# Optimization experiments

Hardware: AMD Instinct MI355X
Metric: run time of the kernel (lower is better)

## Reference

```python
import jax, jax.numpy as jnp
import numpy as np

KNOTS = 17  # integration points on [0, 3]


def _buffers():
    t = jnp.linspace(0.0, 3.0, KNOTS, dtype=jnp.float32)
    dt = 3.0 / (KNOTS - 1)
    w = jnp.full((KNOTS,), 2.0 * dt, dtype=jnp.float32)
    w = w.at[0].set(dt).at[-1].set(dt)          # trapezoid-style end weights
    phi = jnp.exp(-jnp.square(t) / 2.0)         # ideal Gaussian ECF
    return t, phi, w * phi


def setup_inputs() -> dict:
    key = jax.random.key(0)
    k1, k2 = jax.random.split(key)
    N, D, P = 8192, 512, 1024
    z = jax.random.normal(k1, (N, D), dtype=jnp.float32)
    A = jax.random.normal(k2, (D, P), dtype=jnp.float32)  # random projections (hoisted from forward)
    return {"z": z, "A": A}


def reference(z, A):
    t, phi, weights = _buffers()
    D = z.shape[-1]
    flat = z.reshape(-1, D).astype(jnp.float32)            # [N, D]
    An = A / jnp.clip(jnp.linalg.norm(A, axis=0, keepdims=True), 1e-8)
    proj = flat @ An                                       # [N, P]
    x_t = proj[:, :, None] * t                             # [N, P, K]
    cos_mean = jnp.mean(jnp.cos(x_t), axis=0)              # [P, K]
    sin_mean = jnp.mean(jnp.sin(x_t), axis=0)              # [P, K]
    err = jnp.square(cos_mean - phi) + jnp.square(sin_mean)
    statistic = (err @ weights) * flat.shape[0]            # [P]
    return jnp.mean(statistic)
```

## Files before the change

### kernel.cpp

```cpp
#include <hip/hip_runtime.h>
#include <stdint.h>

#define N_SAMP 8192
#define D_DIM  512
#define P_DIM  1024
#define DT     0.1875f

typedef float f32x4 __attribute__((ext_vector_type(4)));
typedef float f32x2 __attribute__((ext_vector_type(2)));
typedef short bf16x8 __attribute__((ext_vector_type(8)));
typedef unsigned short u16;

__device__ __forceinline__ u16 f2bf(float x){
    unsigned int u = __float_as_uint(x);
    return (u16)((u + 0x7FFFu + ((u >> 16) & 1u)) >> 16);
}

__device__ __forceinline__ void load_lds16(const void* g, void* l){
    __builtin_amdgcn_global_load_lds(
        (const __attribute__((address_space(1))) void*)(uintptr_t)g,
        (__attribute__((address_space(3))) void*)(uint32_t)(uintptr_t)l,
        16, 0, 0);
}

__global__ __launch_bounds__(256) void k_prep0(const float4* __restrict__ z4,
                                               u16* __restrict__ zb,
                                               const float* __restrict__ A,
                                               float* __restrict__ inv,
                                               float* __restrict__ out){
    const int tid = threadIdx.x;
    if (blockIdx.x < 4096){
        int i = blockIdx.x * 256 + tid;
        if (i == 0) out[0] = 0.f;
        float4 v = z4[i];
        ushort4 o;
        o.x = f2bf(v.x); o.y = f2bf(v.y); o.z = f2bf(v.z); o.w = f2bf(v.w);
        ((ushort4*)zb)[i] = o;
        return;
    }
    __shared__ float red[8][32];
    const int p0 = (blockIdx.x - 4096) * 32;
    const int pl = tid & 31, dg = tid >> 5;
    float s = 0.f;
    #pragma unroll 8
    for (int i = 0; i < 64; ++i){
        float v = A[(size_t)(dg + 8 * i) * P_DIM + p0 + pl];
        s += v * v;
    }
    red[dg][pl] = s;
    __syncthreads();
    if (tid < 32){
        float t = 0.f;
        #pragma unroll
        for (int g = 0; g < 8; ++g) t += red[g][tid];
        inv[p0 + tid] = 1.0f / fmaxf(sqrtf(t), 1e-8f);
    }
}

__global__ __launch_bounds__(256) void k_trans(const float* __restrict__ A,
                                               const float* __restrict__ inv,
                                               u16* __restrict__ AnT){
    __shared__ float tile[32][33];
    int p0 = (blockIdx.x & 31) * 32;
    int d0 = (blockIdx.x >> 5) * 32;
    int tx = threadIdx.x & 31, ty = threadIdx.x >> 5;
    #pragma unroll
    for (int j = 0; j < 4; ++j){
        int dd = ty + j * 8;
        tile[dd][tx] = A[(size_t)(d0 + dd) * P_DIM + p0 + tx];
    }
    __syncthreads();
    #pragma unroll
    for (int j = 0; j < 4; ++j){
        int pp = ty + j * 8;
        float s = inv[p0 + pp];
        AnT[(size_t)(p0 + pp) * D_DIM + d0 + tx] = f2bf(tile[tx][pp] * s);
    }
}

__global__ __launch_bounds__(256) void k_gemm_ecf(const u16* __restrict__ zb,
                                                  const u16* __restrict__ AnT,
                                                  float* __restrict__ partial){
    __shared__ uint4 smem4[4096];
    const int tid = threadIdx.x;
    const int swz = (blockIdx.x & 7) * 64 + (blockIdx.x >> 3);
    const int bm = swz >> 3, bn = swz & 7;
    const int m0 = bm << 7, n0 = bn << 7;
    const int w = tid >> 6, lane = tid & 63;
    const int r = lane & 15, kg = lane >> 4;
    const int wm = (w >> 1) << 6, wn = (w & 1) << 6;

    const int srow = tid >> 3;
    const int gsw  = ((tid & 7) ^ (srow & 7)) << 3;
    const u16* gA = zb  + (size_t)(m0 + srow) * D_DIM + gsw;
    const u16* gB = AnT + (size_t)(n0 + srow) * D_DIM + gsw;
    char* lbase = (char*)smem4 + w * 1024;

    f32x4 acc[4][4] = {};

    #pragma unroll
    for (int i = 0; i < 4; ++i){
        load_lds16(gA + (size_t)i * 32 * D_DIM, lbase + i * 4096);
        load_lds16(gB + (size_t)i * 32 * D_DIM, lbase + 16384 + i * 4096);
    }

    for (int kt = 0; kt < 8; ++kt){
        const int cur = kt & 1;
        __syncthreads();
        if (kt < 7){
            char* la = lbase + ((kt + 1) & 1) * 32768;
            #pragma unroll
            for (int i = 0; i < 4; ++i){
                load_lds16(gA + (size_t)i * 32 * D_DIM + (kt + 1) * 64, la + i * 4096);
                load_lds16(gB + (size_t)i * 32 * D_DIM + (kt + 1) * 64, la + 16384 + i * 4096);
            }
        }
        const u16* Ab = (const u16*)smem4 + cur * 16384;
        const u16* Bb = Ab + 8192;
        #pragma unroll
        for (int ks = 0; ks < 2; ++ks){
            bf16x8 af[4], bfr[4];
            #pragma unroll
            for (int i = 0; i < 4; ++i)
                af[i] = *(const bf16x8*)&Ab[(wm + i * 16 + r) * 64 +
                                            (((ks * 4 + kg) ^ (r & 7)) << 3)];
            #pragma unroll
            for (int j = 0; j < 4; ++j)
                bfr[j] = *(const bf16x8*)&Bb[(wn + j * 16 + r) * 64 +
                                             (((ks * 4 + kg) ^ (r & 7)) << 3)];
            #pragma unroll
            for (int i = 0; i < 4; ++i)
                #pragma unroll
                for (int j = 0; j < 4; ++j)
                    acc[i][j] = __builtin_amdgcn_mfma_f32_16x16x32_bf16(
                        af[i], bfr[j], acc[i][j], 0, 0, 0);
        }
    }

    __syncthreads();
    float* epil = (float*)smem4;
    #pragma unroll
    for (int jn = 0; jn < 4; ++jn){
        f32x2 sum[16];
        #pragma unroll
        for (int k = 0; k < 16; ++k) sum[k] = (f32x2){0.f, 0.f};
        #pragma unroll
        for (int i = 0; i < 4; ++i){
            #pragma unroll
            for (int q = 0; q < 4; ++q){
                float x = acc[i][jn][q] * DT;
                float c1 = __cosf(x), s1 = __sinf(x);
                float tc = c1 + c1;
                f32x2 prev = {1.f, 0.f};
                f32x2 curv = {c1, s1};
                sum[0] += curv;
                #pragma unroll
                for (int k = 2; k <= 16; ++k){
                    f32x2 nxt = tc * curv - prev;
                    sum[k - 1] += nxt;
                    prev = curv; curv = nxt;
                }
            }
        }
        #pragma unroll
        for (int k = 0; k < 16; ++k){
            f32x2 o;
            o.x = __shfl_xor(sum[k].x, 16); o.y = __shfl_xor(sum[k].y, 16);
            sum[k] += o;
            o.x = __shfl_xor(sum[k].x, 32); o.y = __shfl_xor(sum[k].y, 32);
            sum[k] += o;
        }
        if (lane < 16){
            const int cl = jn * 16 + lane;
            #pragma unroll
            for (int k = 0; k < 16; ++k){
                epil[(w * 32 + k)      * 64 + cl] = sum[k].x;
                epil[(w * 32 + 16 + k) * 64 + cl] = sum[k].y;
            }
        }
    }
    __syncthreads();
    for (int f0 = 0; f0 < 4096; f0 += 256){
        int f = f0 + tid;
        int cl = f & 127, j = f >> 7;
        int whi = cl >> 6, cll = cl & 63;
        float v = epil[(whi * 32 + j) * 64 + cll] +
                  epil[((whi + 2) * 32 + j) * 64 + cll];
        partial[((size_t)bm * 32 + j) * 1024 + n0 + cl] = v;
    }
}

__global__ __launch_bounds__(256) void k_reduce(const float* __restrict__ partial,
                                                float* __restrict__ out){
    const int tid = threadIdx.x;
    const int gt = blockIdx.x * 256 + tid;
    const int pair = gt >> 2, quarter = gt & 3;
    const int p = pair & 1023, j = pair >> 10;
    float s = 0.f;
    #pragma unroll
    for (int i = 0; i < 16; ++i)
        s += partial[((size_t)(quarter * 16 + i) * 32 + j) * 1024 + p];
    s += __shfl_xor(s, 1);
    s += __shfl_xor(s, 2);
    const int k = (j & 15) + 1;
    float tk = (float)k * DT;
    float phik = expf(-0.5f * tk * tk);
    float wk = ((k == 16) ? DT : 2.f * DT) * phik;
    float mean = s * (1.f / (float)N_SAMP);
    float diff = (j < 16) ? (mean - phik) : mean;
    float term = diff * diff * wk;
    #pragma unroll
    for (int o = 32; o > 0; o >>= 1) term += __shfl_xor(term, o);
    __shared__ float red[4];
    if ((tid & 63) == 0) red[tid >> 6] = term;
    __syncthreads();
    if (tid == 0)
        atomicAdd(out, (red[0] + red[1] + red[2] + red[3]) * 0.25f *
                       ((float)N_SAMP / (float)P_DIM));
}

extern "C" void kernel_launch(void* const* d_in, const int* in_sizes, int n_in,
                              void* d_out, int out_size, void* d_ws, size_t ws_size,
                              hipStream_t stream){
    const float* z = (const float*)d_in[0];
    const float* A = (const float*)d_in[1];
    char* ws = (char*)d_ws;
    float* inv     = (float*)(ws);
    u16*   AnT     = (u16*)  (ws + 8192);
    u16*   zb      = (u16*)  (ws + 1056768);
    float* partial = (float*)(ws + 9445376);
    float* out     = (float*)d_out;

    hipLaunchKernelGGL(k_prep0,    dim3(4128), dim3(256), 0, stream,
                       (const float4*)z, zb, A, inv, out);
    hipLaunchKernelGGL(k_trans,    dim3(512),  dim3(256), 0, stream, A, inv, AnT);
    hipLaunchKernelGGL(k_gemm_ecf, dim3(512),  dim3(256), 0, stream, zb, AnT, partial);
    hipLaunchKernelGGL(k_reduce,   dim3(512),  dim3(256), 0, stream, partial, out);
}
```

Before: 50.86 us.

## Fuse prep kernels, defer column scaling to epilogue, reduce partials with atomics

Folds the norm computation, transpose to bf16 and zeroing of the accumulation buffer into one prep launch. The transpose no longer waits on the norms because the per-column inverse norm is now applied in the GEMM epilogue. The per-row-block partial sums are atomically added into a single 32x1024 buffer, so the final reduce reads 128K floats instead of 2M and runs 128 blocks. This removes one launch and a large partial write/read. In exchange it adds atomic contention (64 adders per address), makes the summation order nondeterministic, and bf16-rounds the unnormalized A.

```diff
diff --git a/kernel.cpp b/kernel.cpp
--- a/kernel.cpp
+++ b/kernel.cpp
@@ -23,14 +23,17 @@
         16, 0, 0);
 }
 
-__global__ __launch_bounds__(256) void k_prep0(const float4* __restrict__ z4,
-                                               u16* __restrict__ zb,
-                                               const float* __restrict__ A,
-                                               float* __restrict__ inv,
-                                               float* __restrict__ out){
+__global__ __launch_bounds__(256) void k_prep(const float4* __restrict__ z4,
+                                              u16* __restrict__ zb,
+                                              const float* __restrict__ A,
+                                              float* __restrict__ inv,
+                                              u16* __restrict__ AnT,
+                                              float* __restrict__ gpart,
+                                              float* __restrict__ out){
     const int tid = threadIdx.x;
-    if (blockIdx.x < 4096){
-        int i = blockIdx.x * 256 + tid;
+    const int b = blockIdx.x;
+    if (b < 4096){
+        int i = b * 256 + tid;
         if (i == 0) out[0] = 0.f;
         float4 v = z4[i];
         ushort4 o;
@@ -38,49 +41,50 @@
         ((ushort4*)zb)[i] = o;
         return;
     }
-    __shared__ float red[8][32];
-    const int p0 = (blockIdx.x - 4096) * 32;
-    const int pl = tid & 31, dg = tid >> 5;
-    float s = 0.f;
-    #pragma unroll 8
-    for (int i = 0; i < 64; ++i){
-        float v = A[(size_t)(dg + 8 * i) * P_DIM + p0 + pl];
-        s += v * v;
-    }
-    red[dg][pl] = s;
-    __syncthreads();
-    if (tid < 32){
-        float t = 0.f;
-        #pragma unroll
-        for (int g = 0; g < 8; ++g) t += red[g][tid];
-        inv[p0 + tid] = 1.0f / fmaxf(sqrtf(t), 1e-8f);
-    }
-}
-
-__global__ __launch_bounds__(256) void k_trans(const float* __restrict__ A,
-                                               const float* __restrict__ inv,
-                                               u16* __restrict__ AnT){
-    __shared__ float tile[32][33];
-    int p0 = (blockIdx.x & 31) * 32;
-    int d0 = (blockIdx.x >> 5) * 32;
-    int tx = threadIdx.x & 31, ty = threadIdx.x >> 5;
-    #pragma unroll
-    for (int j = 0; j < 4; ++j){
-        int dd = ty + j * 8;
-        tile[dd][tx] = A[(size_t)(d0 + dd) * P_DIM + p0 + tx];
-    }
-    __syncthreads();
-    #pragma unroll
-    for (int j = 0; j < 4; ++j){
-        int pp = ty + j * 8;
-        float s = inv[p0 + pp];
-        AnT[(size_t)(p0 + pp) * D_DIM + d0 + tx] = f2bf(tile[tx][pp] * s);
-    }
+    if (b < 4128){
+        __shared__ float red[8][32];
+        const int p0 = (b - 4096) * 32;
+        const int pl = tid & 31, dg = tid >> 5;
+        float s = 0.f;
+        #pragma unroll 8
+        for (int i = 0; i < 64; ++i){
+            float v = A[(size_t)(dg + 8 * i) * P_DIM + p0 + pl];
+            s += v * v;
+        }
+        red[dg][pl] = s;
+        __syncthreads();
+        if (tid < 32){
+            float t = 0.f;
+            #pragma unroll
+            for (int g = 0; g < 8; ++g) t += red[g][tid];
+            inv[p0 + tid] = 1.0f / fmaxf(sqrtf(t), 1e-8f);
+        }
+        return;
+    }
+    if (b < 4640){
+        __shared__ float tile[32][33];
+        const int t = b - 4128;
+        const int p0 = (t & 31) * 32, d0 = (t >> 5) * 32;
+        const int tx = tid & 31, ty = tid >> 5;
+        #pragma unroll
+        for (int j = 0; j < 4; ++j)
+            tile[ty + j * 8][tx] = A[(size_t)(d0 + ty + j * 8) * P_DIM + p0 + tx];
+        __syncthreads();
+        #pragma unroll
+        for (int j = 0; j < 4; ++j){
+            int pp = ty + j * 8;
+            AnT[(size_t)(p0 + pp) * D_DIM + d0 + tx] = f2bf(tile[tx][pp]);
+        }
+        return;
+    }
+    int i = (b - 4640) * 256 + tid;
+    ((float4*)gpart)[i] = (float4){0.f, 0.f, 0.f, 0.f};
 }
 
 __global__ __launch_bounds__(256) void k_gemm_ecf(const u16* __restrict__ zb,
                                                   const u16* __restrict__ AnT,
-                                                  float* __restrict__ partial){
+                                                  const float* __restrict__ inv,
+                                                  float* __restrict__ gpart){
     __shared__ uint4 smem4[4096];
     const int tid = threadIdx.x;
     const int swz = (blockIdx.x & 7) * 64 + (blockIdx.x >> 3);
@@ -141,6 +145,7 @@
     float* epil = (float*)smem4;
     #pragma unroll
     for (int jn = 0; jn < 4; ++jn){
+        const float sc = inv[n0 + wn + jn * 16 + r] * DT;
         f32x2 sum[16];
         #pragma unroll
         for (int k = 0; k < 16; ++k) sum[k] = (f32x2){0.f, 0.f};
@@ -148,7 +153,7 @@
         for (int i = 0; i < 4; ++i){
             #pragma unroll
             for (int q = 0; q < 4; ++q){
-                float x = acc[i][jn][q] * DT;
+                float x = acc[i][jn][q] * sc;
                 float c1 = __cosf(x), s1 = __sinf(x);
                 float tc = c1 + c1;
                 f32x2 prev = {1.f, 0.f};
@@ -186,22 +191,16 @@
         int whi = cl >> 6, cll = cl & 63;
         float v = epil[(whi * 32 + j) * 64 + cll] +
                   epil[((whi + 2) * 32 + j) * 64 + cll];
-        partial[((size_t)bm * 32 + j) * 1024 + n0 + cl] = v;
-    }
-}
-
-__global__ __launch_bounds__(256) void k_reduce(const float* __restrict__ partial,
+        atomicAdd(&gpart[j * P_DIM + n0 + cl], v);
+    }
+}
+
+__global__ __launch_bounds__(256) void k_reduce(const float* __restrict__ gpart,
                                                 float* __restrict__ out){
     const int tid = threadIdx.x;
-    const int gt = blockIdx.x * 256 + tid;
-    const int pair = gt >> 2, quarter = gt & 3;
-    const int p = pair & 1023, j = pair >> 10;
-    float s = 0.f;
-    #pragma unroll
-    for (int i = 0; i < 16; ++i)
-        s += partial[((size_t)(quarter * 16 + i) * 32 + j) * 1024 + p];
-    s += __shfl_xor(s, 1);
-    s += __shfl_xor(s, 2);
+    const int idx = blockIdx.x * 256 + tid;
+    const int j = idx >> 10;
+    float s = gpart[idx];
     const int k = (j & 15) + 1;
     float tk = (float)k * DT;
     float phik = expf(-0.5f * tk * tk);
@@ -215,7 +214,7 @@
     if ((tid & 63) == 0) red[tid >> 6] = term;
     __syncthreads();
     if (tid == 0)
-        atomicAdd(out, (red[0] + red[1] + red[2] + red[3]) * 0.25f *
+        atomicAdd(out, (red[0] + red[1] + red[2] + red[3]) *
                        ((float)N_SAMP / (float)P_DIM));
 }
 
@@ -225,15 +224,15 @@
     const float* z = (const float*)d_in[0];
     const float* A = (const float*)d_in[1];
     char* ws = (char*)d_ws;
-    float* inv     = (float*)(ws);
-    u16*   AnT     = (u16*)  (ws + 8192);
-    u16*   zb      = (u16*)  (ws + 1056768);
-    float* partial = (float*)(ws + 9445376);
-    float* out     = (float*)d_out;
-
-    hipLaunchKernelGGL(k_prep0,    dim3(4128), dim3(256), 0, stream,
-                       (const float4*)z, zb, A, inv, out);
-    hipLaunchKernelGGL(k_trans,    dim3(512),  dim3(256), 0, stream, A, inv, AnT);
-    hipLaunchKernelGGL(k_gemm_ecf, dim3(512),  dim3(256), 0, stream, zb, AnT, partial);
-    hipLaunchKernelGGL(k_reduce,   dim3(512),  dim3(256), 0, stream, partial, out);
-}
+    float* inv   = (float*)(ws);
+    float* gpart = (float*)(ws + 8192);
+    u16*   AnT   = (u16*)  (ws + 139264);
+    u16*   zb    = (u16*)  (ws + 1187840);
+    float* out   = (float*)d_out;
+
+    hipLaunchKernelGGL(k_prep,     dim3(4672), dim3(256), 0, stream,
+                       (const float4*)z, zb, A, inv, AnT, gpart, out);
+    hipLaunchKernelGGL(k_gemm_ecf, dim3(512),  dim3(256), 0, stream,
+                       zb, AnT, inv, gpart);
+    hipLaunchKernelGGL(k_reduce,   dim3(128),  dim3(256), 0, stream, gpart, out);
+}
```

Measured after the change: 43.71 us. 14.0% less time.
